# Optimization experiments

Measured on AMD Instinct MI355X. Metric: run time of the kernel, lower is better.

## Reference

```python
import jax, jax.numpy as jnp
import numpy as np

N, C, R = 100000, 128, 3
NUM_EMB = 3  # ceil((r+1)/2)+1 for r=3
E0, EL = 300000, 80000
SC = 0.05


def setup_inputs() -> dict:
    key = jax.random.key(0)
    ks = jax.random.split(key, 40)
    d = {}
    d["x"] = jax.random.normal(ks[0], (N, C), jnp.float32)
    # loopyN0: row 0 = sorted target node ids (CSR requirement), row 1 = neighbor ids
    t0 = jnp.sort(jax.random.randint(ks[1], (E0,), 0, N))
    s0 = jax.random.randint(ks[2], (E0,), 0, N)
    d["loopyN0"] = jnp.stack([t0, s0]).astype(jnp.int32)
    for L in range(1, R + 1):
        tgt = jnp.sort(jax.random.randint(ks[2 + 2 * L], (EL,), 0, N))
        rest = jax.random.randint(ks[3 + 2 * L], (L + 1, EL), 0, N)
        d[f"loopyN{L}"] = jnp.concatenate([tgt[None], rest]).astype(jnp.int32)
        d[f"loopyA{L}"] = jax.random.randint(ks[10 + L], (L + 2, EL), 0, NUM_EMB).astype(jnp.int32)
    # per-conv params (r=3 unshared CustomGINConv layers), stacked on leading axis
    d["emb"] = jax.random.normal(ks[20], (R, NUM_EMB, C)) * SC
    d["Wt"] = jax.random.normal(ks[21], (R, 2 * C, C)) * SC
    d["bt"] = jax.random.normal(ks[22], (R, C)) * SC
    d["mlp_w0"] = jax.random.normal(ks[23], (R, C, C)) * SC
    d["mlp_b0"] = jax.random.normal(ks[24], (R, C)) * SC
    d["mlp_w1"] = jax.random.normal(ks[25], (R, C, C)) * SC
    d["mlp_b1"] = jax.random.normal(ks[26], (R, C)) * SC
    d["conv_eps"] = jnp.ones((R,), jnp.float32)   # CustomGINConv eps init = ones(1)
    d["r_eps"] = jnp.zeros((R + 1,), jnp.float32)
    d["eps"] = jnp.zeros((), jnp.float32)
    # conv_final: MLP(C, C, num_layers=2, norm=Identity, relu)
    d["fin_w0"] = jax.random.normal(ks[27], (C, C)) * SC
    d["fin_b0"] = jax.random.normal(ks[28], (C,)) * SC
    d["fin_w1"] = jax.random.normal(ks[29], (C, C)) * SC
    d["fin_b1"] = jax.random.normal(ks[30], (C,)) * SC
    return d


def _mlp2(h, w0, b0, w1, b1):
    # MLP with num_layers=2, norm=Identity, relu
    h = h @ w0 + b0
    h = jax.nn.relu(h)
    return h @ w1 + b1


def reference(x, loopyN0, loopyN1, loopyN2, loopyN3, loopyA1, loopyA2, loopyA3,
              emb, Wt, bt, mlp_w0, mlp_b0, mlp_w1, mlp_b1,
              conv_eps, r_eps, eps, fin_w0, fin_b0, fin_w1, fin_b1):
    loopyN = [loopyN0, loopyN1, loopyN2, loopyN3]
    loopyA = [None, loopyA1, loopyA2, loopyA3]
    n_nodes = x.shape[0]
    # L = 0: plain neighbor sum (segment_csr over sorted targets == segment_sum)
    seg = jax.ops.segment_sum(x[loopyN0[1]], loopyN0[0], num_segments=n_nodes)
    rc = (1.0 + r_eps[0]) * seg
    for L in range(1, R + 1):
        nl = loopyN[L]
        cc = x[nl[1:]]                                  # [L+1, E, C] path-node gather
        at = loopyA[L][1:]                              # [L+1, E] atomic types
        i = L - 1
        h = jnp.concatenate([cc, emb[i][at]], axis=-1) @ Wt[i] + bt[i]   # [L+1, E, C]
        # custom_propagate: kernel [1,0,1] along path axis, zero 'same' padding
        hp = jnp.pad(h, ((1, 1), (0, 0), (0, 0)))
        y = hp[:-2] + hp[2:]
        o = _mlp2((1.0 + conv_eps[i]) * cc + y, mlp_w0[i], mlp_b0[i], mlp_w1[i], mlp_b1[i])
        o = o.sum(0)                                    # sum over path positions -> [E, C]
        seg = jax.ops.segment_sum(o, nl[0], num_segments=n_nodes)
        rc = rc + (1.0 + r_eps[L]) * seg
    return _mlp2((1.0 + eps) * x + rc, fin_w0, fin_b0, fin_w1, fin_b1)
```

## Files before the change

### kernel.cpp

```cpp
#include <hip/hip_runtime.h>
#include <stdint.h>

#define CDIM 128
#define NNODES 100000
#define E0EDGES 300000
#define ELEDGES 80000

typedef unsigned short u16;
typedef unsigned int u32;
typedef short bf16x8 __attribute__((ext_vector_type(8)));
typedef float f32x4 __attribute__((ext_vector_type(4)));

__device__ __forceinline__ float bf2f(u32 u){
  union { u32 i; float f; } v; v.i = u << 16; return v.f;
}
__device__ __forceinline__ float bf2f_hi(u32 u){
  union { u32 i; float f; } v; v.i = u & 0xffff0000u; return v.f;
}
__device__ __forceinline__ u16 f2bf(float f){
  u32 u = __builtin_bit_cast(u32, f);
  u32 r = (u + 0x7fffu + ((u >> 16) & 1u)) >> 16;
  return (u16)r;
}
__device__ __forceinline__ u32 pack2(float lo, float hi){
  return ((u32)f2bf(hi) << 16) | (u32)f2bf(lo);
}
__device__ __forceinline__ u32 cvtpk(float lo, float hi){
  u32 r;
  asm("v_cvt_pk_bf16_f32 %0, %1, %2" : "=v"(r) : "v"(lo), "v"(hi));
  return r;
}
template<int CTRL>
__device__ __forceinline__ float dppf(float v){
  int r = __builtin_amdgcn_update_dpp(0, __builtin_bit_cast(int, v), CTRL, 0xF, 0xF, true);
  return __builtin_bit_cast(float, r);
}
#define DPP_SHR1 0x111
#define DPP_SHL1 0x101
#define DPP_XOR1 0xB1
#define DPP_XOR2 0x4E

__device__ __forceinline__ void gll16(const void* g, void* l){
  __builtin_amdgcn_global_load_lds(
      (const __attribute__((address_space(1))) void*)g,
      (__attribute__((address_space(3))) void*)l, 16, 0, 0);
}

__device__ __forceinline__ int swzi(int r, int c){
  return r*CDIM + ((((c>>3) ^ (r&7)))<<3) + (c&7);
}
__device__ __forceinline__ int swz8(int r, int col0){
  int chunk = col0 >> 3;
  return r*CDIM + ((chunk ^ (r & 7)) << 3) + (col0 & 7);
}

__device__ __forceinline__ void gemmT(const u16* W, const u16* A, f32x4 acc[2][4],
                                      int rowbase, int featbase, int lr, int g){
#pragma unroll
  for (int ks = 0; ks < 4; ++ks){
    const int sch = ((ks*4 + g) ^ (lr & 7)) << 3;
    bf16x8 a0 = *(const bf16x8*)&A[(rowbase      + lr)*CDIM + sch];
    bf16x8 a1 = *(const bf16x8*)&A[(rowbase + 16 + lr)*CDIM + sch];
    bf16x8 w0f = *(const bf16x8*)&W[(featbase      + lr)*CDIM + sch];
    bf16x8 w1f = *(const bf16x8*)&W[(featbase + 16 + lr)*CDIM + sch];
    bf16x8 w2f = *(const bf16x8*)&W[(featbase + 32 + lr)*CDIM + sch];
    bf16x8 w3f = *(const bf16x8*)&W[(featbase + 48 + lr)*CDIM + sch];
    acc[0][0] = __builtin_amdgcn_mfma_f32_16x16x32_bf16(w0f, a0, acc[0][0], 0, 0, 0);
    acc[0][1] = __builtin_amdgcn_mfma_f32_16x16x32_bf16(w1f, a0, acc[0][1], 0, 0, 0);
    acc[0][2] = __builtin_amdgcn_mfma_f32_16x16x32_bf16(w2f, a0, acc[0][2], 0, 0, 0);
    acc[0][3] = __builtin_amdgcn_mfma_f32_16x16x32_bf16(w3f, a0, acc[0][3], 0, 0, 0);
    acc[1][0] = __builtin_amdgcn_mfma_f32_16x16x32_bf16(w0f, a1, acc[1][0], 0, 0, 0);
    acc[1][1] = __builtin_amdgcn_mfma_f32_16x16x32_bf16(w1f, a1, acc[1][1], 0, 0, 0);
    acc[1][2] = __builtin_amdgcn_mfma_f32_16x16x32_bf16(w2f, a1, acc[1][2], 0, 0, 0);
    acc[1][3] = __builtin_amdgcn_mfma_f32_16x16x32_bf16(w3f, a1, acc[1][3], 0, 0, 0);
  }
}

__device__ __forceinline__ void gemm64(const u16* A, const u16* B, f32x4* acc, int wave, int lane){
  const int lr = lane & 15, g = lane >> 4;
  const int arow = wave*16 + lr;
#pragma unroll
  for (int ks = 0; ks < 4; ++ks){
    const int ach = ks*4 + g;
    bf16x8 a = *(const bf16x8*)&A[arow*CDIM + ((ach ^ (arow & 7)) << 3)];
#pragma unroll
    for (int ct = 0; ct < 8; ++ct){
      const int brow = ct*16 + lr;
      bf16x8 b = *(const bf16x8*)&B[brow*CDIM + ((ach ^ (brow & 7)) << 3)];
      acc[ct] = __builtin_amdgcn_mfma_f32_16x16x32_bf16(a, b, acc[ct], 0, 0, 0);
    }
  }
}

__device__ __forceinline__ void stage_w(const u16* __restrict__ gsrc, u16* sdst, int tid){
  for (int c = tid; c < CDIM*16; c += 256){
    int r = c >> 4, ch = c & 15;
    *(uint4*)&sdst[(r*16 + (ch ^ (r & 7)))*8] = ((const uint4*)(gsrc + r*CDIM))[ch];
  }
}

__global__ __launch_bounds__(256) void prep_aux_kernel(
    const float* __restrict__ x, u16* __restrict__ xb,
    const int* __restrict__ n0, const int* __restrict__ n1,
    const int* __restrict__ n2, const int* __restrict__ n3,
    int* __restrict__ rp0, int* __restrict__ rp1,
    int* __restrict__ rp2, int* __restrict__ rp3,
    const float* __restrict__ Wt, const float* __restrict__ w0, const float* __restrict__ w1,
    const float* __restrict__ fw0, const float* __restrict__ fw1,
    const float* __restrict__ emb, const float* __restrict__ bt,
    u16* __restrict__ WtS, u16* __restrict__ w0S, u16* __restrict__ w1S,
    u16* __restrict__ fw0T, u16* __restrict__ fw1T, float* __restrict__ eWt,
    u16* __restrict__ zrow)
{
  const int XBQ  = NNODES*CDIM/4;
  const int NCSR = E0EDGES + 3*ELEDGES;
  const int NW   = 3*CDIM*CDIM;
  const int NF   = CDIM*CDIM;
  const int NE   = 3*3*CDIM;
  int t = blockIdx.x*256 + threadIdx.x;
  if (t < XBQ){
    size_t idx = (size_t)t*4;
    float4 v = *(const float4*)(x + idx);
    uint2 o; o.x = cvtpk(v.x, v.y); o.y = cvtpk(v.z, v.w);
    *(uint2*)(xb + idx) = o;
    return;
  }
  t -= XBQ;
  if (t < NCSR){
    const int* tgt; int ne; int* rowptr;
    if (t < E0EDGES){ tgt = n0; ne = E0EDGES; rowptr = rp0; }
    else { t -= E0EDGES;
      if (t < ELEDGES){ tgt = n1; ne = ELEDGES; rowptr = rp1; }
      else { t -= ELEDGES;
        if (t < ELEDGES){ tgt = n2; ne = ELEDGES; rowptr = rp2; }
        else { t -= ELEDGES; tgt = n3; ne = ELEDGES; rowptr = rp3; }
      }
    }
    int e = t;
    int tc = tgt[e];
    int tp = (e == 0) ? -1 : tgt[e-1];
    for (int n = tp + 1; n <= tc; ++n) rowptr[n] = e;
    if (e == ne - 1){
      for (int n = tc + 1; n <= NNODES; ++n) rowptr[n] = ne;
    }
    return;
  }
  t -= NCSR;
  if (t < NW){
    int i = t >> 14, s = t & 16383;
    int r = s >> 7, ch = ((s >> 3) & 15) ^ (r & 7), k = ch*8 + (s & 7);
    WtS[t] = f2bf(Wt[(size_t)i*2*CDIM*CDIM + k*CDIM + r]);
    w0S[t] = f2bf(w0[(size_t)i*CDIM*CDIM + k*CDIM + r]);
    w1S[t] = f2bf(w1[(size_t)i*CDIM*CDIM + k*CDIM + r]);
    return;
  }
  t -= NW;
  if (t < NF){
    int col = t/CDIM, k = t%CDIM;
    fw0T[t] = f2bf(fw0[k*CDIM + col]);
    fw1T[t] = f2bf(fw1[k*CDIM + col]);
    return;
  }
  t -= NF;
  if (t < NE){
    int i = t/(3*CDIM), a = (t/CDIM)%3, c2 = t%CDIM;
    float s = bt[i*CDIM + c2];
    for (int k = 0; k < CDIM; ++k)
      s += emb[(i*3 + a)*CDIM + k] * Wt[(size_t)i*2*CDIM*CDIM + (CDIM + k)*CDIM + c2];
    eWt[t] = s;
    return;
  }
  t -= NE;
  if (t < 64) ((u32*)zrow)[t] = 0u;
}

template<int L>
__device__ __forceinline__ void layer_body(
    int bidx,
    const u16* __restrict__ xb,
    const int* __restrict__ nl, const int* __restrict__ ai,
    const u16* __restrict__ WtS, const u16* __restrict__ w0S, const u16* __restrict__ w1S,
    const float* __restrict__ eWt,
    const float* __restrict__ b0g, const float* __restrict__ b1g,
    const float* __restrict__ cepsg,
    const u16* __restrict__ zrow,
    u16* __restrict__ oL,
    u16* sW, u16* sA, float* sE, float* b0s, float* b1s, int* sAid)
{
  constexpr int RPE = (L == 1) ? 2 : 4;
  constexpr int TE  = 128 / RPE;
  constexpr int LI  = L - 1;

  const int tid  = threadIdx.x;
  const int wave = tid >> 6, lane = tid & 63;
  const int lr   = lane & 15, g = lane >> 4;
  const int wr   = wave >> 1, wc = wave & 1;
  const int rowbase  = wr*32;
  const int featbase = wc*64;
  const int e0   = bidx * TE;
  const int pos  = lr & (RPE - 1);
  const float mu = (pos > 0) ? 1.f : 0.f;
  const float md = (pos < L) ? 1.f : 0.f;
  const float mz = (L == 2 && pos == 3) ? 0.f : 1.f;
  const float ce = 1.0f + cepsg[LI];

  {
    const u16* src = WtS + LI*CDIM*CDIM + wave*4*512 + lane*8;
    u16* dst = sW + wave*4*512;
#pragma unroll
    for (int j = 0; j < 4; ++j) gll16(src + j*512, dst + j*512);
  }
#pragma unroll
  for (int i = 0; i < 4; ++i){
    const int r  = wave*16 + 4*i + (lane >> 4);
    const int p  = r & (RPE - 1);
    const int pc = (p <= L) ? p : 0;
    const int node = nl[(1 + pc)*ELEDGES + e0 + r/RPE];
    const u16* src = (p <= L) ? (xb + (size_t)node*CDIM) : zrow;
    const int cl = lane & 15;
    gll16(src + ((cl ^ (r & 7)) << 3), sA + (wave*16 + 4*i)*CDIM);
  }
  for (int c = tid; c < 3*CDIM; c += 512) sE[(c>>7)*136 + (c&127)] = eWt[LI*3*CDIM + c];
  if (tid < CDIM) b0s[tid] = b0g[LI*CDIM + tid];
  else if (tid < 2*CDIM) b1s[tid-CDIM] = b1g[LI*CDIM + (tid-CDIM)];
  if (tid < 128){
    int p = tid & (RPE - 1);
    sAid[tid] = (p <= L) ? ai[(1 + p)*ELEDGES + e0 + tid/RPE] : 0;
  }
  __syncthreads();

  f32x4 acc[2][4];
#pragma unroll
  for (int a = 0; a < 2; ++a)
#pragma unroll
    for (int b = 0; b < 4; ++b) acc[a][b] = (f32x4){0.f,0.f,0.f,0.f};
  __builtin_amdgcn_s_setprio(1);
  gemmT(sW, sA, acc, rowbase, featbase, lr, g);
  __builtin_amdgcn_s_setprio(0);
  __syncthreads();

  {
    const u16* src = w0S + LI*CDIM*CDIM + wave*4*512 + lane*8;
    u16* dst = sW + wave*4*512;
#pragma unroll
    for (int j = 0; j < 4; ++j) gll16(src + j*512, dst + j*512);
  }
#pragma unroll
  for (int a = 0; a < 2; ++a){
    const int r = rowbase + 16*a + lr;
    const float* eWrow = &sE[sAid[r]*136];
#pragma unroll
    for (int b = 0; b < 4; ++b){
      const int col0 = featbase + 16*b + g*4;
      float4 ew = *(const float4*)&eWrow[col0];
      float h0 = acc[a][b][0] + ew.x;
      float h1 = acc[a][b][1] + ew.y;
      float h2 = acc[a][b][2] + ew.z;
      float h3 = acc[a][b][3] + ew.w;
      float u0 = dppf<DPP_SHR1>(h0), u1 = dppf<DPP_SHR1>(h1),
            u2 = dppf<DPP_SHR1>(h2), u3 = dppf<DPP_SHR1>(h3);
      float d0 = dppf<DPP_SHL1>(h0), d1 = dppf<DPP_SHL1>(h1),
            d2 = dppf<DPP_SHL1>(h2), d3 = dppf<DPP_SHL1>(h3);
      uint2 ccv = *(const uint2*)&sA[swz8(r, col0)];
      float c0 = bf2f(ccv.x & 0xffffu), c1 = bf2f_hi(ccv.x);
      float c2 = bf2f(ccv.y & 0xffffu), c3 = bf2f_hi(ccv.y);
      uint2 zv;
      zv.x = cvtpk(ce*c0 + mu*u0 + md*d0, ce*c1 + mu*u1 + md*d1);
      zv.y = cvtpk(ce*c2 + mu*u2 + md*d2, ce*c3 + mu*u3 + md*d3);
      *(uint2*)&sA[swz8(r, col0)] = zv;
    }
  }
  __syncthreads();

#pragma unroll
  for (int a = 0; a < 2; ++a)
#pragma unroll
    for (int b = 0; b < 4; ++b) acc[a][b] = (f32x4){0.f,0.f,0.f,0.f};
  __builtin_amdgcn_s_setprio(1);
  gemmT(sW, sA, acc, rowbase, featbase, lr, g);
  __builtin_amdgcn_s_setprio(0);
  __syncthreads();

  {
    const u16* src = w1S + LI*CDIM*CDIM + wave*4*512 + lane*8;
    u16* dst = sW + wave*4*512;
#pragma unroll
    for (int j = 0; j < 4; ++j) gll16(src + j*512, dst + j*512);
  }
#pragma unroll
  for (int a = 0; a < 2; ++a){
    const int r = rowbase + 16*a + lr;
#pragma unroll
    for (int b = 0; b < 4; ++b){
      const int col0 = featbase + 16*b + g*4;
      float4 bb = *(const float4*)&b0s[col0];
      float t0 = acc[a][b][0] + bb.x; t0 = t0 > 0.f ? t0 : 0.f;
      float t1 = acc[a][b][1] + bb.y; t1 = t1 > 0.f ? t1 : 0.f;
      float t2 = acc[a][b][2] + bb.z; t2 = t2 > 0.f ? t2 : 0.f;
      float t3 = acc[a][b][3] + bb.w; t3 = t3 > 0.f ? t3 : 0.f;
      uint2 tv; tv.x = cvtpk(t0, t1); tv.y = cvtpk(t2, t3);
      *(uint2*)&sA[swz8(r, col0)] = tv;
    }
  }
  __syncthreads();

#pragma unroll
  for (int a = 0; a < 2; ++a)
#pragma unroll
    for (int b = 0; b < 4; ++b) acc[a][b] = (f32x4){0.f,0.f,0.f,0.f};
  __builtin_amdgcn_s_setprio(1);
  gemmT(sW, sA, acc, rowbase, featbase, lr, g);
  __builtin_amdgcn_s_setprio(0);

  const float nb = (float)(L + 1);
#pragma unroll
  for (int a = 0; a < 2; ++a){
    const int r = rowbase + 16*a + lr;
    const int ed = e0 + r/RPE;
#pragma unroll
    for (int b = 0; b < 4; ++b){
      float v0 = mz*acc[a][b][0], v1 = mz*acc[a][b][1],
            v2 = mz*acc[a][b][2], v3 = mz*acc[a][b][3];
      v0 += dppf<DPP_XOR1>(v0); v1 += dppf<DPP_XOR1>(v1);
      v2 += dppf<DPP_XOR1>(v2); v3 += dppf<DPP_XOR1>(v3);
      if constexpr (RPE == 4){
        v0 += dppf<DPP_XOR2>(v0); v1 += dppf<DPP_XOR2>(v1);
        v2 += dppf<DPP_XOR2>(v2); v3 += dppf<DPP_XOR2>(v3);
      }
      if (pos == 0){
        const int col0 = featbase + 16*b + g*4;
        float4 bb = *(const float4*)&b1s[col0];
        uint2 ov;
        ov.x = cvtpk(v0 + nb*bb.x, v1 + nb*bb.y);
        ov.y = cvtpk(v2 + nb*bb.z, v3 + nb*bb.w);
        *(uint2*)(oL + (size_t)ed*CDIM + col0) = ov;
      }
    }
  }
}

__global__ __launch_bounds__(512, 4) void layers_kernel(
    const u16* __restrict__ xb,
    const int* __restrict__ n1, const int* __restrict__ a1,
    const int* __restrict__ n2, const int* __restrict__ a2,
    const int* __restrict__ n3, const int* __restrict__ a3,
    const u16* __restrict__ WtS, const u16* __restrict__ w0S, const u16* __restrict__ w1S,
    const float* __restrict__ eWt,
    const float* __restrict__ b0g, const float* __restrict__ b1g,
    const float* __restrict__ cepsg,
    const u16* __restrict__ zrow,
    u16* __restrict__ o1, u16* __restrict__ o2, u16* __restrict__ o3)
{
  __shared__ __align__(16) u16 sW[CDIM*CDIM];
  __shared__ __align__(16) u16 sA[128*CDIM];
  __shared__ __align__(16) float sE[3*136];
  __shared__ __align__(16) float b0s[CDIM];
  __shared__ __align__(16) float b1s[CDIM];
  __shared__ int sAid[128];
  constexpr int NB1 = ELEDGES/64;
  constexpr int NB2 = ELEDGES/32;
  const int b = blockIdx.x;
  if (b < NB1)
    layer_body<1>(b, xb, n1, a1, WtS, w0S, w1S, eWt, b0g, b1g, cepsg, zrow, o1,
                  sW, sA, sE, b0s, b1s, sAid);
  else if (b < NB1 + NB2)
    layer_body<2>(b - NB1, xb, n2, a2, WtS, w0S, w1S, eWt, b0g, b1g, cepsg, zrow, o2,
                  sW, sA, sE, b0s, b1s, sAid);
  else
    layer_body<3>(b - NB1 - NB2, xb, n3, a3, WtS, w0S, w1S, eWt, b0g, b1g, cepsg, zrow, o3,
                  sW, sA, sE, b0s, b1s, sAid);
}

__global__ __launch_bounds__(256) void gather_rc_kernel(
    const float* __restrict__ x, const u16* __restrict__ xbopt,
    const int* __restrict__ s0,
    const int* __restrict__ rp0, const int* __restrict__ rp1,
    const int* __restrict__ rp2, const int* __restrict__ rp3,
    const u16* __restrict__ o1, const u16* __restrict__ o2, const u16* __restrict__ o3,
    const float* __restrict__ repsg, u16* __restrict__ rcb)
{
  const int wave = threadIdx.x >> 6, lane = threadIdx.x & 63;
  const int node = blockIdx.x*4 + wave;
  if (node >= NNODES) return;
  if (xbopt){
    const int lr = lane & 15, gg = lane >> 4;
    float a0=0.f,a1=0.f,a2=0.f,a3=0.f,a4=0.f,a5=0.f,a6=0.f,a7=0.f;
    {
      const float sc = 1.f + repsg[0];
      const int lo = rp0[node], hi = rp0[node+1];
      for (int e = lo + gg; e < hi; e += 4){
        int s = s0[e];
        uint4 v = *(const uint4*)(xbopt + (size_t)s*CDIM + lr*8);
        a0 = fmaf(sc, bf2f(v.x & 0xffffu), a0); a1 = fmaf(sc, bf2f_hi(v.x), a1);
        a2 = fmaf(sc, bf2f(v.y & 0xffffu), a2); a3 = fmaf(sc, bf2f_hi(v.y), a3);
        a4 = fmaf(sc, bf2f(v.z & 0xffffu), a4); a5 = fmaf(sc, bf2f_hi(v.z), a5);
        a6 = fmaf(sc, bf2f(v.w & 0xffffu), a6); a7 = fmaf(sc, bf2f_hi(v.w), a7);
      }
    }
    const u16* os[3]  = {o1, o2, o3};
    const int* rps[3] = {rp1, rp2, rp3};
#pragma unroll
    for (int li = 0; li < 3; ++li){
      const float sc = 1.f + repsg[1+li];
      const int lo = rps[li][node], hi = rps[li][node+1];
      const u16* ob = os[li];
      for (int e = lo + gg; e < hi; e += 4){
        uint4 v = *(const uint4*)(ob + (size_t)e*CDIM + lr*8);
        a0 = fmaf(sc, bf2f(v.x & 0xffffu), a0); a1 = fmaf(sc, bf2f_hi(v.x), a1);
        a2 = fmaf(sc, bf2f(v.y & 0xffffu), a2); a3 = fmaf(sc, bf2f_hi(v.y), a3);
        a4 = fmaf(sc, bf2f(v.z & 0xffffu), a4); a5 = fmaf(sc, bf2f_hi(v.z), a5);
        a6 = fmaf(sc, bf2f(v.w & 0xffffu), a6); a7 = fmaf(sc, bf2f_hi(v.w), a7);
      }
    }
    a0 += __shfl_xor(a0, 16, 64); a1 += __shfl_xor(a1, 16, 64);
    a2 += __shfl_xor(a2, 16, 64); a3 += __shfl_xor(a3, 16, 64);
    a4 += __shfl_xor(a4, 16, 64); a5 += __shfl_xor(a5, 16, 64);
    a6 += __shfl_xor(a6, 16, 64); a7 += __shfl_xor(a7, 16, 64);
    a0 += __shfl_xor(a0, 32, 64); a1 += __shfl_xor(a1, 32, 64);
    a2 += __shfl_xor(a2, 32, 64); a3 += __shfl_xor(a3, 32, 64);
    a4 += __shfl_xor(a4, 32, 64); a5 += __shfl_xor(a5, 32, 64);
    a6 += __shfl_xor(a6, 32, 64); a7 += __shfl_xor(a7, 32, 64);
    if (gg == 0){
      uint4 ov;
      ov.x = cvtpk(a0, a1); ov.y = cvtpk(a2, a3);
      ov.z = cvtpk(a4, a5); ov.w = cvtpk(a6, a7);
      *(uint4*)(rcb + (size_t)node*CDIM + lr*8) = ov;
    }
  } else {
    float a0 = 0.f, a1 = 0.f;
    {
      const float sc = 1.f + repsg[0];
      int lo = rp0[node], hi = rp0[node+1];
      for (int e = lo; e < hi; ++e){
        int s = s0[e];
        float2 v = *(const float2*)(x + (size_t)s*CDIM + lane*2);
        a0 += sc*v.x; a1 += sc*v.y;
      }
    }
    const u16* os[3]  = {o1, o2, o3};
    const int* rps[3] = {rp1, rp2, rp3};
#pragma unroll
    for (int li = 0; li < 3; ++li){
      const float sc = 1.f + repsg[1+li];
      int lo = rps[li][node], hi = rps[li][node+1];
      for (int e = lo; e < hi; ++e){
        u32 v = *(const u32*)(os[li] + (size_t)e*CDIM + lane*2);
        a0 += sc*bf2f(v & 0xffffu); a1 += sc*bf2f_hi(v);
      }
    }
    *(u32*)(rcb + (size_t)node*CDIM + lane*2) = pack2(a0, a1);
  }
}

__global__ __launch_bounds__(256) void final_kernel(
    const float* __restrict__ x, const u16* __restrict__ xbopt,
    const u16* __restrict__ rc,
    const u16* __restrict__ fw0T, const u16* __restrict__ fw1T,
    const float* __restrict__ fb0, const float* __restrict__ fb1,
    const float* __restrict__ epsg, float* __restrict__ outp)
{
  __shared__ __align__(16) u16 sW[CDIM*CDIM];
  __shared__ __align__(16) u16 sA[64*CDIM];
  const int tid  = threadIdx.x;
  const int wave = tid >> 6, lane = tid & 63;
  const int lr   = lane & 15, g = lane >> 4;
  const int r0   = blockIdx.x * 64;
  const float se = 1.0f + epsg[0];

  stage_w(fw0T, sW, tid);
  for (int c = tid; c < 64*16; c += 256){
    int r = c >> 4, ch = c & 15;
    int node = r0 + r;
    uint4 v = make_uint4(0,0,0,0);
    if (node < NNODES){
      const u32* pr = (const u32*)(rc + (size_t)node*CDIM + ch*8);
      u32 r0v = pr[0], r1v = pr[1], r2v = pr[2], r3v = pr[3];
      if (xbopt){
        uint4 xv = *(const uint4*)(xbopt + (size_t)node*CDIM + ch*8);
        v.x = cvtpk(se*bf2f(xv.x & 0xffffu) + bf2f(r0v & 0xffffu), se*bf2f_hi(xv.x) + bf2f_hi(r0v));
        v.y = cvtpk(se*bf2f(xv.y & 0xffffu) + bf2f(r1v & 0xffffu), se*bf2f_hi(xv.y) + bf2f_hi(r1v));
        v.z = cvtpk(se*bf2f(xv.z & 0xffffu) + bf2f(r2v & 0xffffu), se*bf2f_hi(xv.z) + bf2f_hi(r2v));
        v.w = cvtpk(se*bf2f(xv.w & 0xffffu) + bf2f(r3v & 0xffffu), se*bf2f_hi(xv.w) + bf2f_hi(r3v));
      } else {
        const float4* px = (const float4*)(x + (size_t)node*CDIM + ch*8);
        float4 fa = px[0], fb = px[1];
        v.x = pack2(se*fa.x + bf2f(r0v & 0xffffu), se*fa.y + bf2f_hi(r0v));
        v.y = pack2(se*fa.z + bf2f(r1v & 0xffffu), se*fa.w + bf2f_hi(r1v));
        v.z = pack2(se*fb.x + bf2f(r2v & 0xffffu), se*fb.y + bf2f_hi(r2v));
        v.w = pack2(se*fb.z + bf2f(r3v & 0xffffu), se*fb.w + bf2f_hi(r3v));
      }
    }
    *(uint4*)&sA[(r*16 + (ch ^ (r & 7)))*8] = v;
  }
  __syncthreads();

  f32x4 acc[8];
#pragma unroll
  for (int ct = 0; ct < 8; ++ct) acc[ct] = (f32x4){0.f,0.f,0.f,0.f};
  gemm64(sA, sW, acc, wave, lane);
  __syncthreads();
#pragma unroll
  for (int ct = 0; ct < 8; ++ct){
    const int col = ct*16 + lr;
    const float bb = fb0[col];
#pragma unroll
    for (int q = 0; q < 4; ++q){
      const int r = wave*16 + g*4 + q;
      float t = acc[ct][q] + bb;
      t = t > 0.f ? t : 0.f;
      sA[swzi(r, col)] = f2bf(t);
    }
  }
  stage_w(fw1T, sW, tid);
  __syncthreads();
#pragma unroll
  for (int ct = 0; ct < 8; ++ct) acc[ct] = (f32x4){0.f,0.f,0.f,0.f};
  gemm64(sA, sW, acc, wave, lane);
#pragma unroll
  for (int ct = 0; ct < 8; ++ct){
    const int col = ct*16 + lr;
    const float bb = fb1[col];
#pragma unroll
    for (int q = 0; q < 4; ++q){
      const int r = wave*16 + g*4 + q;
      int node = r0 + r;
      if (node < NNODES) outp[(size_t)node*CDIM + col] = acc[ct][q] + bb;
    }
  }
}

extern "C" void kernel_launch(void* const* d_in, const int* in_sizes, int n_in,
                              void* d_out, int out_size, void* d_ws, size_t ws_size,
                              hipStream_t stream)
{
  const float* x   = (const float*)d_in[0];
  const int* n0    = (const int*)d_in[1];
  const int* n1    = (const int*)d_in[2];
  const int* a1    = (const int*)d_in[3];
  const int* n2    = (const int*)d_in[4];
  const int* a2    = (const int*)d_in[5];
  const int* n3    = (const int*)d_in[6];
  const int* a3    = (const int*)d_in[7];
  const float* emb = (const float*)d_in[8];
  const float* Wt  = (const float*)d_in[9];
  const float* bt  = (const float*)d_in[10];
  const float* w0  = (const float*)d_in[11];
  const float* b0  = (const float*)d_in[12];
  const float* w1  = (const float*)d_in[13];
  const float* b1  = (const float*)d_in[14];
  const float* ceps= (const float*)d_in[15];
  const float* reps= (const float*)d_in[16];
  const float* eps = (const float*)d_in[17];
  const float* fw0 = (const float*)d_in[18];
  const float* fb0 = (const float*)d_in[19];
  const float* fw1 = (const float*)d_in[20];
  const float* fb1 = (const float*)d_in[21];
  float* outp = (float*)d_out;

  char* w = (char*)d_ws;
  size_t off = 0;
  auto alloc = [&](size_t bytes) -> char* {
    char* p = w + off;
    off += (bytes + 255) & ~((size_t)255);
    return p;
  };
  u16* o1   = (u16*)alloc((size_t)ELEDGES*CDIM*2);
  u16* o2   = (u16*)alloc((size_t)ELEDGES*CDIM*2);
  u16* o3   = (u16*)alloc((size_t)ELEDGES*CDIM*2);
  u16* rcb  = (u16*)alloc((size_t)NNODES*CDIM*2);
  int* rp0  = (int*)alloc((size_t)(NNODES+1)*4);
  int* rp1  = (int*)alloc((size_t)(NNODES+1)*4);
  int* rp2  = (int*)alloc((size_t)(NNODES+1)*4);
  int* rp3  = (int*)alloc((size_t)(NNODES+1)*4);
  u16* WtS  = (u16*)alloc((size_t)3*CDIM*CDIM*2);
  u16* w0S  = (u16*)alloc((size_t)3*CDIM*CDIM*2);
  u16* w1S  = (u16*)alloc((size_t)3*CDIM*CDIM*2);
  u16* fw0T = (u16*)alloc((size_t)CDIM*CDIM*2);
  u16* fw1T = (u16*)alloc((size_t)CDIM*CDIM*2);
  float* eWt = (float*)alloc((size_t)3*3*CDIM*4);
  u16* zrow = (u16*)alloc((size_t)CDIM*2);
  const size_t xbbytes = (size_t)NNODES*CDIM*2;
  u16* xb; const u16* xbopt;
  if (off + xbbytes <= ws_size){ xb = (u16*)alloc(xbbytes); xbopt = xb; }
  else { xb = rcb; xbopt = nullptr; }
  (void)in_sizes; (void)n_in; (void)out_size;

  {
    const int XBQ = NNODES*CDIM/4;
    int total = XBQ + (E0EDGES + 3*ELEDGES) + 3*CDIM*CDIM + CDIM*CDIM + 3*3*CDIM + 64;
    prep_aux_kernel<<<(total + 255)/256, 256, 0, stream>>>(
        x, xb, n0, n1, n2, n3, rp0, rp1, rp2, rp3,
        Wt, w0, w1, fw0, fw1, emb, bt,
        WtS, w0S, w1S, fw0T, fw1T, eWt, zrow);
  }

  layers_kernel<<<ELEDGES/64 + 2*(ELEDGES/32), 512, 0, stream>>>(
      xb, n1, a1, n2, a2, n3, a3, WtS, w0S, w1S, eWt, b0, b1, ceps, zrow, o1, o2, o3);

  gather_rc_kernel<<<(NNODES+3)/4, 256, 0, stream>>>(x, xbopt, n0 + E0EDGES, rp0, rp1, rp2, rp3,
                                                     o1, o2, o3, reps, rcb);
  final_kernel<<<(NNODES+63)/64, 256, 0, stream>>>(x, xbopt, rcb, fw0T, fw1T, fb0, fb1, eps, outp);
}
```

Measured before the change: 362.2 us.

## Enlarge per-wave MFMA tile to 64x64 with 256-thread blocks; unroll gather loops

The layers kernel drops from 8 waves to 4 waves per block, so each wave computes a 64x64 output tile (4x4 MFMA accumulators) instead of 32x64. Staging of weights and gathered rows is redistributed to match. Each wave now reuses more operand fragments per LDS read, at the cost of more accumulator registers and fewer waves to hide latency. Separately, the gather_rc loops are unrolled by two so two independent row loads are in flight per iteration.

```diff
diff --git a/kernel.cpp b/kernel.cpp
--- a/kernel.cpp
+++ b/kernel.cpp
@@ -54,25 +54,23 @@
   return r*CDIM + ((chunk ^ (r & 7)) << 3) + (col0 & 7);
 }
 
-__device__ __forceinline__ void gemmT(const u16* W, const u16* A, f32x4 acc[2][4],
+__device__ __forceinline__ void gemm4(const u16* W, const u16* A, f32x4 acc[4][4],
                                       int rowbase, int featbase, int lr, int g){
 #pragma unroll
   for (int ks = 0; ks < 4; ++ks){
     const int sch = ((ks*4 + g) ^ (lr & 7)) << 3;
-    bf16x8 a0 = *(const bf16x8*)&A[(rowbase      + lr)*CDIM + sch];
-    bf16x8 a1 = *(const bf16x8*)&A[(rowbase + 16 + lr)*CDIM + sch];
-    bf16x8 w0f = *(const bf16x8*)&W[(featbase      + lr)*CDIM + sch];
-    bf16x8 w1f = *(const bf16x8*)&W[(featbase + 16 + lr)*CDIM + sch];
-    bf16x8 w2f = *(const bf16x8*)&W[(featbase + 32 + lr)*CDIM + sch];
-    bf16x8 w3f = *(const bf16x8*)&W[(featbase + 48 + lr)*CDIM + sch];
-    acc[0][0] = __builtin_amdgcn_mfma_f32_16x16x32_bf16(w0f, a0, acc[0][0], 0, 0, 0);
-    acc[0][1] = __builtin_amdgcn_mfma_f32_16x16x32_bf16(w1f, a0, acc[0][1], 0, 0, 0);
-    acc[0][2] = __builtin_amdgcn_mfma_f32_16x16x32_bf16(w2f, a0, acc[0][2], 0, 0, 0);
-    acc[0][3] = __builtin_amdgcn_mfma_f32_16x16x32_bf16(w3f, a0, acc[0][3], 0, 0, 0);
-    acc[1][0] = __builtin_amdgcn_mfma_f32_16x16x32_bf16(w0f, a1, acc[1][0], 0, 0, 0);
-    acc[1][1] = __builtin_amdgcn_mfma_f32_16x16x32_bf16(w1f, a1, acc[1][1], 0, 0, 0);
-    acc[1][2] = __builtin_amdgcn_mfma_f32_16x16x32_bf16(w2f, a1, acc[1][2], 0, 0, 0);
-    acc[1][3] = __builtin_amdgcn_mfma_f32_16x16x32_bf16(w3f, a1, acc[1][3], 0, 0, 0);
+    bf16x8 af[4], wf[4];
+#pragma unroll
+    for (int a = 0; a < 4; ++a)
+      af[a] = *(const bf16x8*)&A[(rowbase + 16*a + lr)*CDIM + sch];
+#pragma unroll
+    for (int b = 0; b < 4; ++b)
+      wf[b] = *(const bf16x8*)&W[(featbase + 16*b + lr)*CDIM + sch];
+#pragma unroll
+    for (int a = 0; a < 4; ++a)
+#pragma unroll
+      for (int b = 0; b < 4; ++b)
+        acc[a][b] = __builtin_amdgcn_mfma_f32_16x16x32_bf16(wf[b], af[a], acc[a][b], 0, 0, 0);
   }
 }
 
@@ -194,9 +192,8 @@
   const int tid  = threadIdx.x;
   const int wave = tid >> 6, lane = tid & 63;
   const int lr   = lane & 15, g = lane >> 4;
-  const int wr   = wave >> 1, wc = wave & 1;
-  const int rowbase  = wr*32;
-  const int featbase = wc*64;
+  const int rowbase  = (wave >> 1)*64;
+  const int featbase = (wave & 1)*64;
   const int e0   = bidx * TE;
   const int pos  = lr & (RPE - 1);
   const float mu = (pos > 0) ? 1.f : 0.f;
@@ -205,22 +202,21 @@
   const float ce = 1.0f + cepsg[LI];
 
   {
-    const u16* src = WtS + LI*CDIM*CDIM + wave*4*512 + lane*8;
-    u16* dst = sW + wave*4*512;
-#pragma unroll
-    for (int j = 0; j < 4; ++j) gll16(src + j*512, dst + j*512);
-  }
-#pragma unroll
-  for (int i = 0; i < 4; ++i){
-    const int r  = wave*16 + 4*i + (lane >> 4);
+    const u16* src = WtS + LI*CDIM*CDIM + wave*8*512 + lane*8;
+    u16* dst = sW + wave*8*512;
+#pragma unroll
+    for (int j = 0; j < 8; ++j) gll16(src + j*512, dst + j*512);
+  }
+#pragma unroll
+  for (int i = 0; i < 8; ++i){
+    const int r  = wave*32 + 4*i + (lane >> 4);
     const int p  = r & (RPE - 1);
     const int pc = (p <= L) ? p : 0;
     const int node = nl[(1 + pc)*ELEDGES + e0 + r/RPE];
     const u16* src = (p <= L) ? (xb + (size_t)node*CDIM) : zrow;
-    const int cl = lane & 15;
-    gll16(src + ((cl ^ (r & 7)) << 3), sA + (wave*16 + 4*i)*CDIM);
-  }
-  for (int c = tid; c < 3*CDIM; c += 512) sE[(c>>7)*136 + (c&127)] = eWt[LI*3*CDIM + c];
+    gll16(src + (((lane & 15) ^ (r & 7)) << 3), sA + (wave*32 + 4*i)*CDIM);
+  }
+  for (int c = tid; c < 3*CDIM; c += 256) sE[(c>>7)*136 + (c&127)] = eWt[LI*3*CDIM + c];
   if (tid < CDIM) b0s[tid] = b0g[LI*CDIM + tid];
   else if (tid < 2*CDIM) b1s[tid-CDIM] = b1g[LI*CDIM + (tid-CDIM)];
   if (tid < 128){
@@ -229,24 +225,24 @@
   }
   __syncthreads();
 
-  f32x4 acc[2][4];
-#pragma unroll
-  for (int a = 0; a < 2; ++a)
+  f32x4 acc[4][4];
+#pragma unroll
+  for (int a = 0; a < 4; ++a)
 #pragma unroll
     for (int b = 0; b < 4; ++b) acc[a][b] = (f32x4){0.f,0.f,0.f,0.f};
   __builtin_amdgcn_s_setprio(1);
-  gemmT(sW, sA, acc, rowbase, featbase, lr, g);
+  gemm4(sW, sA, acc, rowbase, featbase, lr, g);
   __builtin_amdgcn_s_setprio(0);
   __syncthreads();
 
   {
-    const u16* src = w0S + LI*CDIM*CDIM + wave*4*512 + lane*8;
-    u16* dst = sW + wave*4*512;
-#pragma unroll
-    for (int j = 0; j < 4; ++j) gll16(src + j*512, dst + j*512);
-  }
-#pragma unroll
-  for (int a = 0; a < 2; ++a){
+    const u16* src = w0S + LI*CDIM*CDIM + wave*8*512 + lane*8;
+    u16* dst = sW + wave*8*512;
+#pragma unroll
+    for (int j = 0; j < 8; ++j) gll16(src + j*512, dst + j*512);
+  }
+#pragma unroll
+  for (int a = 0; a < 4; ++a){
     const int r = rowbase + 16*a + lr;
     const float* eWrow = &sE[sAid[r]*136];
 #pragma unroll
@@ -273,22 +269,22 @@
   __syncthreads();
 
 #pragma unroll
-  for (int a = 0; a < 2; ++a)
+  for (int a = 0; a < 4; ++a)
 #pragma unroll
     for (int b = 0; b < 4; ++b) acc[a][b] = (f32x4){0.f,0.f,0.f,0.f};
   __builtin_amdgcn_s_setprio(1);
-  gemmT(sW, sA, acc, rowbase, featbase, lr, g);
+  gemm4(sW, sA, acc, rowbase, featbase, lr, g);
   __builtin_amdgcn_s_setprio(0);
   __syncthreads();
 
   {
-    const u16* src = w1S + LI*CDIM*CDIM + wave*4*512 + lane*8;
-    u16* dst = sW + wave*4*512;
-#pragma unroll
-    for (int j = 0; j < 4; ++j) gll16(src + j*512, dst + j*512);
-  }
-#pragma unroll
-  for (int a = 0; a < 2; ++a){
+    const u16* src = w1S + LI*CDIM*CDIM + wave*8*512 + lane*8;
+    u16* dst = sW + wave*8*512;
+#pragma unroll
+    for (int j = 0; j < 8; ++j) gll16(src + j*512, dst + j*512);
+  }
+#pragma unroll
+  for (int a = 0; a < 4; ++a){
     const int r = rowbase + 16*a + lr;
 #pragma unroll
     for (int b = 0; b < 4; ++b){
@@ -305,16 +301,16 @@
   __syncthreads();
 
 #pragma unroll
-  for (int a = 0; a < 2; ++a)
+  for (int a = 0; a < 4; ++a)
 #pragma unroll
     for (int b = 0; b < 4; ++b) acc[a][b] = (f32x4){0.f,0.f,0.f,0.f};
   __builtin_amdgcn_s_setprio(1);
-  gemmT(sW, sA, acc, rowbase, featbase, lr, g);
+  gemm4(sW, sA, acc, rowbase, featbase, lr, g);
   __builtin_amdgcn_s_setprio(0);
 
   const float nb = (float)(L + 1);
 #pragma unroll
-  for (int a = 0; a < 2; ++a){
+  for (int a = 0; a < 4; ++a){
     const int r = rowbase + 16*a + lr;
     const int ed = e0 + r/RPE;
 #pragma unroll
@@ -339,7 +335,7 @@
   }
 }
 
-__global__ __launch_bounds__(512, 4) void layers_kernel(
+__global__ __launch_bounds__(256, 2) void layers_kernel(
     const u16* __restrict__ xb,
     const int* __restrict__ n1, const int* __restrict__ a1,
     const int* __restrict__ n2, const int* __restrict__ a2,
@@ -388,7 +384,21 @@
     {
       const float sc = 1.f + repsg[0];
       const int lo = rp0[node], hi = rp0[node+1];
-      for (int e = lo + gg; e < hi; e += 4){
+      int e = lo + gg;
+      for (; e + 4 < hi; e += 8){
+        int s1 = s0[e], s2 = s0[e+4];
+        uint4 v = *(const uint4*)(xbopt + (size_t)s1*CDIM + lr*8);
+        uint4 w = *(const uint4*)(xbopt + (size_t)s2*CDIM + lr*8);
+        a0 = fmaf(sc, bf2f(v.x & 0xffffu), a0); a1 = fmaf(sc, bf2f_hi(v.x), a1);
+        a2 = fmaf(sc, bf2f(v.y & 0xffffu), a2); a3 = fmaf(sc, bf2f_hi(v.y), a3);
+        a4 = fmaf(sc, bf2f(v.z & 0xffffu), a4); a5 = fmaf(sc, bf2f_hi(v.z), a5);
+        a6 = fmaf(sc, bf2f(v.w & 0xffffu), a6); a7 = fmaf(sc, bf2f_hi(v.w), a7);
+        a0 = fmaf(sc, bf2f(w.x & 0xffffu), a0); a1 = fmaf(sc, bf2f_hi(w.x), a1);
+        a2 = fmaf(sc, bf2f(w.y & 0xffffu), a2); a3 = fmaf(sc, bf2f_hi(w.y), a3);
+        a4 = fmaf(sc, bf2f(w.z & 0xffffu), a4); a5 = fmaf(sc, bf2f_hi(w.z), a5);
+        a6 = fmaf(sc, bf2f(w.w & 0xffffu), a6); a7 = fmaf(sc, bf2f_hi(w.w), a7);
+      }
+      if (e < hi){
         int s = s0[e];
         uint4 v = *(const uint4*)(xbopt + (size_t)s*CDIM + lr*8);
         a0 = fmaf(sc, bf2f(v.x & 0xffffu), a0); a1 = fmaf(sc, bf2f_hi(v.x), a1);
@@ -404,7 +414,20 @@
       const float sc = 1.f + repsg[1+li];
       const int lo = rps[li][node], hi = rps[li][node+1];
       const u16* ob = os[li];
-      for (int e = lo + gg; e < hi; e += 4){
+      int e = lo + gg;
+      for (; e + 4 < hi; e += 8){
+        uint4 v = *(const uint4*)(ob + (size_t)e*CDIM + lr*8);
+        uint4 w = *(const uint4*)(ob + (size_t)(e+4)*CDIM + lr*8);
+        a0 = fmaf(sc, bf2f(v.x & 0xffffu), a0); a1 = fmaf(sc, bf2f_hi(v.x), a1);
+        a2 = fmaf(sc, bf2f(v.y & 0xffffu), a2); a3 = fmaf(sc, bf2f_hi(v.y), a3);
+        a4 = fmaf(sc, bf2f(v.z & 0xffffu), a4); a5 = fmaf(sc, bf2f_hi(v.z), a5);
+        a6 = fmaf(sc, bf2f(v.w & 0xffffu), a6); a7 = fmaf(sc, bf2f_hi(v.w), a7);
+        a0 = fmaf(sc, bf2f(w.x & 0xffffu), a0); a1 = fmaf(sc, bf2f_hi(w.x), a1);
+        a2 = fmaf(sc, bf2f(w.y & 0xffffu), a2); a3 = fmaf(sc, bf2f_hi(w.y), a3);
+        a4 = fmaf(sc, bf2f(w.z & 0xffffu), a4); a5 = fmaf(sc, bf2f_hi(w.z), a5);
+        a6 = fmaf(sc, bf2f(w.w & 0xffffu), a6); a7 = fmaf(sc, bf2f_hi(w.w), a7);
+      }
+      if (e < hi){
         uint4 v = *(const uint4*)(ob + (size_t)e*CDIM + lr*8);
         a0 = fmaf(sc, bf2f(v.x & 0xffffu), a0); a1 = fmaf(sc, bf2f_hi(v.x), a1);
         a2 = fmaf(sc, bf2f(v.y & 0xffffu), a2); a3 = fmaf(sc, bf2f_hi(v.y), a3);
@@ -594,7 +617,7 @@
         WtS, w0S, w1S, fw0T, fw1T, eWt, zrow);
   }
 
-  layers_kernel<<<ELEDGES/64 + 2*(ELEDGES/32), 512, 0, stream>>>(
+  layers_kernel<<<ELEDGES/64 + 2*(ELEDGES/32), 256, 0, stream>>>(
       xb, n1, a1, n2, a2, n3, a3, WtS, w0S, w1S, eWt, b0, b1, ceps, zrow, o1, o2, o3);
 
   gather_rc_kernel<<<(NNODES+3)/4, 256, 0, stream>>>(x, xbopt, n0 + E0EDGES, rp0, rp1, rp2, rp3,
```

Measured after the change: 376.3 us. +3.9%, slower.
